# Performance work log

Hardware: AMD Instinct MI355X
Metric: run time of the kernel (lower is better)

The kernel has to match this reference:

```python
import jax, jax.numpy as jnp
import numpy as np

MAX_FREQ = 4
OMEGA = 0.5 * np.pi
PATCH = 64


def _unnorm(c, size):
    # align_corners=False convention of torch.grid_sample
    return ((c + 1.0) * size - 1.0) / 2.0


def _gather(im, yy, xx):
    # im [C,H,W], yy/xx [Ho,Wo] -> [C,Ho,Wo]
    return im[:, yy, xx]


def _gs_nearest(inp, grid):
    # inp [B,C,H,W], grid [B,Ho,Wo,2] (x,y); padding_mode='border'
    B, C, H, W = inp.shape
    x = jnp.clip(jnp.round(_unnorm(grid[..., 0], W)), 0, W - 1).astype(jnp.int32)
    y = jnp.clip(jnp.round(_unnorm(grid[..., 1], H)), 0, H - 1).astype(jnp.int32)
    return jax.vmap(_gather)(inp, y, x)  # [B,C,Ho,Wo]


def _gs_bilinear(inp, grid):
    B, C, H, W = inp.shape
    x = jnp.clip(_unnorm(grid[..., 0], W), 0.0, W - 1.0)
    y = jnp.clip(_unnorm(grid[..., 1], H), 0.0, H - 1.0)
    x0 = jnp.floor(x); y0 = jnp.floor(y)
    wx = (x - x0)[:, None]; wy = (y - y0)[:, None]  # [B,1,Ho,Wo]
    x0i = x0.astype(jnp.int32); y0i = y0.astype(jnp.int32)
    x1i = jnp.minimum(x0i + 1, W - 1); y1i = jnp.minimum(y0i + 1, H - 1)
    g = jax.vmap(_gather)
    v00 = g(inp, y0i, x0i); v01 = g(inp, y0i, x1i)
    v10 = g(inp, y1i, x0i); v11 = g(inp, y1i, x1i)
    return (v00 * (1 - wx) * (1 - wy) + v01 * wx * (1 - wy)
            + v10 * (1 - wx) * wy + v11 * wx * wy)


def _conv2d(x, w, b):
    y = jax.lax.conv_general_dilated(x, w, (1, 1), ((1, 1), (1, 1)),
                                     dimension_numbers=("NCHW", "OIHW", "NCHW"))
    return y + b[None, :, None, None]


def _lc_decoder(q, rel):
    # q [B,Ho,Wo,2F+1], rel [B,Ho,Wo,1]; Fourier basis [1, cos(k*w*rel), sin(k*w*rel)]
    k = jnp.arange(1, MAX_FREQ + 1, dtype=q.dtype)
    ang = rel * k * OMEGA  # [B,Ho,Wo,F]
    basis = jnp.concatenate([jnp.ones_like(rel), jnp.cos(ang), jnp.sin(ang)], axis=-1)
    return jnp.sum(q * basis, axis=-1, keepdims=True)  # [B,Ho,Wo,1]


def _forward(sinogram, feat, grid, square_inv, adapt_w, adapt_b):
    B = feat.shape[0]
    sino = _conv2d(feat, adapt_w, adapt_b)          # [B,2F+1,V,D]
    V, D = sino.shape[-2], sino.shape[-1]
    # make_coord along detector axis (dim=1 coord channel), padding=0
    coord_d = ((jnp.arange(D, dtype=sino.dtype) + 0.5) / D) * 2.0 - 1.0
    sino_coord = jnp.broadcast_to(coord_d[None, None, None, :], (B, 1, V, D))
    shift_interval = 1.0 / D
    eps = 1e-4
    q_recons, lengths = [], []
    for sx in (-shift_interval, shift_interval):  # ensembling shifts
        g = grid + jnp.array([sx, 0.0], dtype=grid.dtype) + 1e-6
        q_recon = jnp.transpose(_gs_nearest(sino, g), (0, 2, 3, 1))       # [B,V,P2,2F+1]
        q_coord = jnp.transpose(_gs_nearest(sino_coord, g), (0, 2, 3, 1))  # [B,V,P2,1]
        rel = (grid[..., 0:1] - q_coord) * D
        q_recons.append(_lc_decoder(q_recon, rel))
        lengths.append(jnp.abs(rel) + eps)
    tot = lengths[0] + lengths[1]
    # lengths are swapped before weighting (cross weighting)
    recon = q_recons[0] * lengths[1] / tot + q_recons[1] * lengths[0] / tot
    out = jnp.sum(jnp.transpose(recon, (0, 3, 1, 2)) * square_inv * 10000.0, axis=-2)
    # back projection of center channel of raw sinogram
    ch = sinogram.shape[1]
    bp = _gs_bilinear(sinogram[:, ch // 2:ch // 2 + 1], grid)
    out = out + jnp.sum(bp * square_inv * 10000.0, axis=-2)  # [B,1,P2]
    return out.reshape(B, 1, PATCH, PATCH)


def setup_inputs() -> dict:
    key = jax.random.key(0)
    ks = jax.random.split(key, 6)
    B, V, D, ENC = 4, 360, 512, 64
    P2 = PATCH * PATCH
    CH = 2 * MAX_FREQ + 1
    return {
        "sinogram": jax.random.normal(ks[0], (B, 1, V, D), jnp.float32),
        "feat": jax.random.normal(ks[1], (B, ENC, V, D), jnp.float32),
        "grid": jax.random.uniform(ks[2], (B, V, P2, 2), jnp.float32, -1.0, 1.0),
        "square_inv": jax.random.uniform(ks[3], (B, 1, V, P2), jnp.float32, 1e-5, 1e-4),
        "adapt_w": jax.random.normal(ks[4], (CH, ENC, 3, 3), jnp.float32) * 0.05,
        "adapt_b": jax.random.normal(ks[5], (CH,), jnp.float32) * 0.05,
    }


def reference(sinogram, feat, grid, square_inv, adapt_w, adapt_b):
    return _forward(sinogram, feat, grid, square_inv, adapt_w, adapt_b)
```

## Files before the change

kernel.cpp:

```cpp
#include <hip/hip_runtime.h>
#include <math.h>

#define B   4
#define V   360
#define D   512
#define ENC 64
#define CH  9
#define P2  4096
#define NCHUNK 24
#define VCHUNK 15
#define DPT 4

template <int SS>
__global__ __launch_bounds__(256) void conv_kernel(
    const float* __restrict__ feat,
    const float* __restrict__ w,
    const float* __restrict__ bias,
    float* __restrict__ sino)
{
    const int bid = blockIdx.x;
    const int sw  = (bid & 7) * 90 + (bid >> 3);
    const int b   = sw / 180;
    const int vt  = sw % 180;
    const int tr  = threadIdx.x >> 7;
    const int v   = vt * 2 + tr;
    const int d0  = (threadIdx.x & 127) * DPT;

    float acc[CH][DPT];
    #pragma unroll
    for (int oc = 0; oc < CH; ++oc) {
        const float bv = bias[oc];
        #pragma unroll
        for (int p = 0; p < DPT; ++p) acc[oc][p] = bv;
    }

    const float* fb = feat + ((size_t)b * ENC * V + v) * D + d0;
    const bool vm = v > 0, vp = v < V - 1;
    const bool dm = d0 > 0, dp = (d0 + DPT) < D;

    for (int ic = 0; ic < ENC; ++ic) {
        const float* f = fb + (size_t)ic * (V * D);
        float r[3][DPT + 2];
        #pragma unroll
        for (int rr = 0; rr < 3; ++rr) {
            const float* fr = f + (rr - 1) * D;
            const bool ok = (rr == 0) ? vm : ((rr == 2) ? vp : true);
            float4 c = ok ? *(const float4*)fr : float4{0.f, 0.f, 0.f, 0.f};
            r[rr][1] = c.x; r[rr][2] = c.y; r[rr][3] = c.z; r[rr][4] = c.w;
            r[rr][0] = (ok && dm) ? fr[-1]  : 0.f;
            r[rr][5] = (ok && dp) ? fr[DPT] : 0.f;
        }
        #pragma unroll
        for (int oc = 0; oc < CH; ++oc) {
            const float* ww = w + ((size_t)oc * ENC + ic) * 9;
            #pragma unroll
            for (int kr = 0; kr < 3; ++kr) {
                #pragma unroll
                for (int kc = 0; kc < 3; ++kc) {
                    const float wv = ww[kr * 3 + kc];
                    #pragma unroll
                    for (int p = 0; p < DPT; ++p)
                        acc[oc][p] = fmaf(r[kr][p + kc], wv, acc[oc][p]);
                }
            }
        }
    }

    #pragma unroll
    for (int p = 0; p < DPT; ++p) {
        float* so = sino + (size_t)(((size_t)b * V + v) * D + d0 + p) * SS;
        if (SS == 16) {
            float4* so4 = (float4*)so;
            so4[0] = float4{acc[0][p], acc[1][p], acc[2][p], acc[3][p]};
            so4[1] = float4{acc[4][p], acc[5][p], acc[6][p], acc[7][p]};
            so[8]  = acc[8][p];
        } else {
            #pragma unroll
            for (int oc = 0; oc < CH; ++oc) so[oc] = acc[oc][p];
        }
    }
}

template <int SS>
__global__ __launch_bounds__(256) void sample_kernel(
    const float* __restrict__ sino,
    const float* __restrict__ sinogram,
    const float* __restrict__ grid,
    const float* __restrict__ sq,
    float* __restrict__ partial)
{
    const int p  = blockIdx.x * 256 + threadIdx.x;
    const int v0 = blockIdx.y * VCHUNK;
    const int b  = blockIdx.z;

    const float* sg = sinogram + (size_t)b * V * D;
    const float* sb = sino + (size_t)b * V * D * SS;

    float acc = 0.f;
    for (int v = v0; v < v0 + VCHUNK; ++v) {
        const size_t gi = (size_t)(b * V + v) * P2 + p;
        const float gx = grid[gi * 2 + 0];
        const float gy = grid[gi * 2 + 1];
        const float s  = sq[gi];

        float fy = ((gy + 1e-6f + 1.f) * (float)V - 1.f) * 0.5f;
        int   yi = (int)fminf(fmaxf(rintf(fy), 0.f), (float)(V - 1));

        float val[2], len[2];
        #pragma unroll
        for (int sft = 0; sft < 2; ++sft) {
            const float sxv = (sft == 0) ? (-1.f / (float)D) : (1.f / (float)D);
            float fx = ((gx + sxv + 1e-6f + 1.f) * (float)D - 1.f) * 0.5f;
            int   xi = (int)fminf(fmaxf(rintf(fx), 0.f), (float)(D - 1));
            float qc = ((float)xi + 0.5f) * (2.f / (float)D) - 1.f;
            float rel = (gx - qc) * (float)D;

            float q[9];
            const float* qp = sb + (size_t)(yi * D + xi) * SS;
            if (SS == 16) {
                const float4* q4 = (const float4*)qp;
                float4 a = q4[0], c = q4[1];
                q[0] = a.x; q[1] = a.y; q[2] = a.z; q[3] = a.w;
                q[4] = c.x; q[5] = c.y; q[6] = c.z; q[7] = c.w;
                q[8] = qp[8];
            } else {
                #pragma unroll
                for (int k = 0; k < 9; ++k) q[k] = qp[k];
            }

            const float ang = rel * 1.5707963267948966f;
            float s1, c1;
            __sincosf(ang, &s1, &c1);
            const float c2 = fmaf(2.f * c1, c1, -1.f);
            const float s2 = 2.f * c1 * s1;
            const float c3 = fmaf(2.f * c1, c2, -c1);
            const float s3 = fmaf(2.f * c1, s2, -s1);
            const float c4 = fmaf(2.f * c1, c3, -c2);
            const float s4 = fmaf(2.f * c1, s3, -s2);

            float vv = q[0];
            vv = fmaf(q[1], c1, vv); vv = fmaf(q[2], c2, vv);
            vv = fmaf(q[3], c3, vv); vv = fmaf(q[4], c4, vv);
            vv = fmaf(q[5], s1, vv); vv = fmaf(q[6], s2, vv);
            vv = fmaf(q[7], s3, vv); vv = fmaf(q[8], s4, vv);
            val[sft] = vv;
            len[sft] = fabsf(rel) + 1e-4f;
        }
        const float tot   = len[0] + len[1];
        const float recon = (val[0] * len[1] + val[1] * len[0]) / tot;

        float fxb = fminf(fmaxf(((gx + 1.f) * (float)D - 1.f) * 0.5f, 0.f), (float)(D - 1));
        float fyb = fminf(fmaxf(((gy + 1.f) * (float)V - 1.f) * 0.5f, 0.f), (float)(V - 1));
        float x0 = floorf(fxb), y0 = floorf(fyb);
        float wx = fxb - x0,    wy = fyb - y0;
        int x0i = (int)x0, y0i = (int)y0;
        int x1i = min(x0i + 1, D - 1), y1i = min(y0i + 1, V - 1);
        float v00 = sg[y0i * D + x0i], v01 = sg[y0i * D + x1i];
        float v10 = sg[y1i * D + x0i], v11 = sg[y1i * D + x1i];
        float bp = v00 * (1.f - wx) * (1.f - wy) + v01 * wx * (1.f - wy)
                 + v10 * (1.f - wx) * wy        + v11 * wx * wy;

        acc += (recon + bp) * s * 1e4f;
    }
    partial[((size_t)blockIdx.y * B + b) * P2 + p] = acc;
}

__global__ __launch_bounds__(256) void reduce_kernel(
    const float* __restrict__ partial, float* __restrict__ out)
{
    const int i = blockIdx.x * 256 + threadIdx.x;
    float a = 0.f;
    #pragma unroll
    for (int c = 0; c < NCHUNK; ++c) a += partial[(size_t)c * B * P2 + i];
    out[i] = a;
}

extern "C" void kernel_launch(void* const* d_in, const int* in_sizes, int n_in,
                              void* d_out, int out_size, void* d_ws, size_t ws_size,
                              hipStream_t stream)
{
    const float* sinogram = (const float*)d_in[0];
    const float* feat     = (const float*)d_in[1];
    const float* grid     = (const float*)d_in[2];
    const float* sq       = (const float*)d_in[3];
    const float* w        = (const float*)d_in[4];
    const float* bias     = (const float*)d_in[5];
    float* out = (float*)d_out;

    const size_t part_bytes = (size_t)NCHUNK * B * P2 * sizeof(float);
    const size_t need16 = (size_t)B * V * D * 16 * sizeof(float) + part_bytes;
    const int ss = (ws_size >= need16) ? 16 : 9;

    float* sino    = (float*)d_ws;
    float* partial = (float*)((char*)d_ws + (size_t)B * V * D * ss * sizeof(float));

    dim3 sgrid(P2 / 256, NCHUNK, B);
    if (ss == 16) {
        conv_kernel<16><<<dim3(720), 256, 0, stream>>>(feat, w, bias, sino);
        sample_kernel<16><<<sgrid, 256, 0, stream>>>(sino, sinogram, grid, sq, partial);
    } else {
        conv_kernel<9><<<dim3(720), 256, 0, stream>>>(feat, w, bias, sino);
        sample_kernel<9><<<sgrid, 256, 0, stream>>>(sino, sinogram, grid, sq, partial);
    }

    reduce_kernel<<<dim3((B * P2) / 256), 256, 0, stream>>>(partial, out);
}
```

Measured before the change: 314.5 us.

## Store conv output as fp16 records and remap sample grid per XCD

The conv kernel now has each thread compute 8 detector columns over 4 views per block, and it writes its 9 channels as packed fp16 in a 32-byte record instead of fp32. The sample kernel reads these half records, loads grid coordinates as a single 64-bit nontemporal load, and processes two views per iteration. It also uses a new block index mapping that keeps each batch on a pair of XCDs, with a smaller view chunk and therefore more partial sums. The goal is to cut gather bandwidth and cache pressure in the sampling stage and raise parallelism. The cost is lower precision of the intermediate sinogram features, which could affect accuracy tolerance.

```diff
diff --git a/kernel.cpp b/kernel.cpp
--- a/kernel.cpp
+++ b/kernel.cpp
@@ -1,4 +1,5 @@
 #include <hip/hip_runtime.h>
+#include <hip/hip_fp16.h>
 #include <math.h>
 
 #define B   4
@@ -7,24 +8,24 @@
 #define ENC 64
 #define CH  9
 #define P2  4096
-#define NCHUNK 24
-#define VCHUNK 15
-#define DPT 4
-
-template <int SS>
+#define NCHUNK 45
+#define VCHUNK 8
+#define DPT 8
+#define RECH 16
+
 __global__ __launch_bounds__(256) void conv_kernel(
     const float* __restrict__ feat,
     const float* __restrict__ w,
     const float* __restrict__ bias,
-    float* __restrict__ sino)
+    __half* __restrict__ sino)
 {
     const int bid = blockIdx.x;
-    const int sw  = (bid & 7) * 90 + (bid >> 3);
-    const int b   = sw / 180;
-    const int vt  = sw % 180;
-    const int tr  = threadIdx.x >> 7;
-    const int v   = vt * 2 + tr;
-    const int d0  = (threadIdx.x & 127) * DPT;
+    const int sw  = (bid & 7) * 45 + (bid >> 3);
+    const int b   = sw / 90;
+    const int vt  = sw % 90;
+    const int tr  = threadIdx.x >> 6;
+    const int v   = vt * 4 + tr;
+    const int d0  = (threadIdx.x & 63) * DPT;
 
     float acc[CH][DPT];
     #pragma unroll
@@ -45,10 +46,12 @@
         for (int rr = 0; rr < 3; ++rr) {
             const float* fr = f + (rr - 1) * D;
             const bool ok = (rr == 0) ? vm : ((rr == 2) ? vp : true);
-            float4 c = ok ? *(const float4*)fr : float4{0.f, 0.f, 0.f, 0.f};
-            r[rr][1] = c.x; r[rr][2] = c.y; r[rr][3] = c.z; r[rr][4] = c.w;
-            r[rr][0] = (ok && dm) ? fr[-1]  : 0.f;
-            r[rr][5] = (ok && dp) ? fr[DPT] : 0.f;
+            float4 c0 = ok ? *(const float4*)fr       : float4{0.f, 0.f, 0.f, 0.f};
+            float4 c1 = ok ? *(const float4*)(fr + 4) : float4{0.f, 0.f, 0.f, 0.f};
+            r[rr][1] = c0.x; r[rr][2] = c0.y; r[rr][3] = c0.z; r[rr][4] = c0.w;
+            r[rr][5] = c1.x; r[rr][6] = c1.y; r[rr][7] = c1.z; r[rr][8] = c1.w;
+            r[rr][0]       = (ok && dm) ? fr[-1]   : 0.f;
+            r[rr][DPT + 1] = (ok && dp) ? fr[DPT]  : 0.f;
         }
         #pragma unroll
         for (int oc = 0; oc < CH; ++oc) {
@@ -68,101 +71,123 @@
 
     #pragma unroll
     for (int p = 0; p < DPT; ++p) {
-        float* so = sino + (size_t)(((size_t)b * V + v) * D + d0 + p) * SS;
-        if (SS == 16) {
-            float4* so4 = (float4*)so;
-            so4[0] = float4{acc[0][p], acc[1][p], acc[2][p], acc[3][p]};
-            so4[1] = float4{acc[4][p], acc[5][p], acc[6][p], acc[7][p]};
-            so[8]  = acc[8][p];
-        } else {
-            #pragma unroll
-            for (int oc = 0; oc < CH; ++oc) so[oc] = acc[oc][p];
-        }
-    }
-}
-
-template <int SS>
+        __half* rec = sino + (size_t)(((size_t)b * V + v) * D + d0 + p) * RECH;
+        union { __half2 h; unsigned u; } cv;
+        uint4 pk;
+        cv.h = __floats2half2_rn(acc[0][p], acc[1][p]); pk.x = cv.u;
+        cv.h = __floats2half2_rn(acc[2][p], acc[3][p]); pk.y = cv.u;
+        cv.h = __floats2half2_rn(acc[4][p], acc[5][p]); pk.z = cv.u;
+        cv.h = __floats2half2_rn(acc[6][p], acc[7][p]); pk.w = cv.u;
+        *(uint4*)rec = pk;
+        cv.h = __floats2half2_rn(acc[8][p], 0.f);
+        *(unsigned*)(rec + 8) = cv.u;
+    }
+}
+
+__device__ __forceinline__ void unpack9(const __half* rec, float* q)
+{
+    const uint4 a = *(const uint4*)rec;
+    union { unsigned u; __half2 h; } c;
+    float2 f;
+    c.u = a.x; f = __half22float2(c.h); q[0] = f.x; q[1] = f.y;
+    c.u = a.y; f = __half22float2(c.h); q[2] = f.x; q[3] = f.y;
+    c.u = a.z; f = __half22float2(c.h); q[4] = f.x; q[5] = f.y;
+    c.u = a.w; f = __half22float2(c.h); q[6] = f.x; q[7] = f.y;
+    const unsigned e = *(const unsigned*)(rec + 8);
+    union { unsigned short us; __half hh; } c2;
+    c2.us = (unsigned short)e;
+    q[8] = __half2float(c2.hh);
+}
+
+__device__ __forceinline__ float point_contrib(
+    int b, int v, int p,
+    const __half* __restrict__ sb, const float* __restrict__ sg,
+    const float* __restrict__ grid, const float* __restrict__ sq)
+{
+    const size_t gi = (size_t)(b * V + v) * P2 + p;
+    const double gd = __builtin_nontemporal_load((const double*)grid + gi);
+    const unsigned long long gu = __double_as_longlong(gd);
+    const float gx = __uint_as_float((unsigned)gu);
+    const float gy = __uint_as_float((unsigned)(gu >> 32));
+    const float s  = __builtin_nontemporal_load(sq + gi);
+
+    const float fy = ((gy + 1e-6f + 1.f) * (float)V - 1.f) * 0.5f;
+    const int   yi = (int)fminf(fmaxf(rintf(fy), 0.f), (float)(V - 1));
+    const float fx0 = ((gx + 1e-6f + 1.f) * (float)D - 1.f) * 0.5f;
+
+    float val[2], len[2];
+    #pragma unroll
+    for (int sft = 0; sft < 2; ++sft) {
+        const float fx = (sft == 0) ? (fx0 - 0.5f) : (fx0 + 0.5f);
+        const int   xi = (int)fminf(fmaxf(rintf(fx), 0.f), (float)(D - 1));
+        const float qc = ((float)xi + 0.5f) * (2.f / (float)D) - 1.f;
+        const float rel = (gx - qc) * (float)D;
+
+        float q[9];
+        unpack9(sb + (size_t)(yi * D + xi) * RECH, q);
+
+        const float ang = rel * 1.5707963267948966f;
+        float s1, c1;
+        __sincosf(ang, &s1, &c1);
+        const float c2 = fmaf(2.f * c1, c1, -1.f);
+        const float s2 = 2.f * c1 * s1;
+        const float c3 = fmaf(2.f * c1, c2, -c1);
+        const float s3 = fmaf(2.f * c1, s2, -s1);
+        const float c4 = fmaf(2.f * c1, c3, -c2);
+        const float s4 = fmaf(2.f * c1, s3, -s2);
+
+        float vv = q[0];
+        vv = fmaf(q[1], c1, vv); vv = fmaf(q[2], c2, vv);
+        vv = fmaf(q[3], c3, vv); vv = fmaf(q[4], c4, vv);
+        vv = fmaf(q[5], s1, vv); vv = fmaf(q[6], s2, vv);
+        vv = fmaf(q[7], s3, vv); vv = fmaf(q[8], s4, vv);
+        val[sft] = vv;
+        len[sft] = fabsf(rel) + 1e-4f;
+    }
+    const float tot   = len[0] + len[1];
+    const float recon = (val[0] * len[1] + val[1] * len[0]) / tot;
+
+    float fxb = fminf(fmaxf(((gx + 1.f) * (float)D - 1.f) * 0.5f, 0.f), (float)(D - 1));
+    float fyb = fminf(fmaxf(((gy + 1.f) * (float)V - 1.f) * 0.5f, 0.f), (float)(V - 1));
+    const float x0 = floorf(fxb), y0 = floorf(fyb);
+    const float wx = fxb - x0,    wy = fyb - y0;
+    const int x0i = (int)x0, y0i = (int)y0;
+    const int x1i = min(x0i + 1, D - 1), y1i = min(y0i + 1, V - 1);
+    const float v00 = sg[y0i * D + x0i], v01 = sg[y0i * D + x1i];
+    const float v10 = sg[y1i * D + x0i], v11 = sg[y1i * D + x1i];
+    const float bp = v00 * (1.f - wx) * (1.f - wy) + v01 * wx * (1.f - wy)
+                   + v10 * (1.f - wx) * wy        + v11 * wx * wy;
+
+    return (recon + bp) * s * 1e4f;
+}
+
 __global__ __launch_bounds__(256) void sample_kernel(
-    const float* __restrict__ sino,
+    const __half* __restrict__ sino,
     const float* __restrict__ sinogram,
     const float* __restrict__ grid,
     const float* __restrict__ sq,
     float* __restrict__ partial)
 {
-    const int p  = blockIdx.x * 256 + threadIdx.x;
-    const int v0 = blockIdx.y * VCHUNK;
-    const int b  = blockIdx.z;
+    const int bid = blockIdx.x;
+    const int xcd = bid & 7;
+    const int b   = xcd >> 1;
+    const int idx = ((bid >> 3) << 1) | (xcd & 1);
+    const int chunk = idx >> 4;
+    const int p  = (idx & 15) * 256 + threadIdx.x;
+    const int v0 = chunk * VCHUNK;
 
     const float* sg = sinogram + (size_t)b * V * D;
-    const float* sb = sino + (size_t)b * V * D * SS;
+    const __half* sb = sino + (size_t)b * V * D * RECH;
 
     float acc = 0.f;
-    for (int v = v0; v < v0 + VCHUNK; ++v) {
-        const size_t gi = (size_t)(b * V + v) * P2 + p;
-        const float gx = grid[gi * 2 + 0];
-        const float gy = grid[gi * 2 + 1];
-        const float s  = sq[gi];
-
-        float fy = ((gy + 1e-6f + 1.f) * (float)V - 1.f) * 0.5f;
-        int   yi = (int)fminf(fmaxf(rintf(fy), 0.f), (float)(V - 1));
-
-        float val[2], len[2];
-        #pragma unroll
-        for (int sft = 0; sft < 2; ++sft) {
-            const float sxv = (sft == 0) ? (-1.f / (float)D) : (1.f / (float)D);
-            float fx = ((gx + sxv + 1e-6f + 1.f) * (float)D - 1.f) * 0.5f;
-            int   xi = (int)fminf(fmaxf(rintf(fx), 0.f), (float)(D - 1));
-            float qc = ((float)xi + 0.5f) * (2.f / (float)D) - 1.f;
-            float rel = (gx - qc) * (float)D;
-
-            float q[9];
-            const float* qp = sb + (size_t)(yi * D + xi) * SS;
-            if (SS == 16) {
-                const float4* q4 = (const float4*)qp;
-                float4 a = q4[0], c = q4[1];
-                q[0] = a.x; q[1] = a.y; q[2] = a.z; q[3] = a.w;
-                q[4] = c.x; q[5] = c.y; q[6] = c.z; q[7] = c.w;
-                q[8] = qp[8];
-            } else {
-                #pragma unroll
-                for (int k = 0; k < 9; ++k) q[k] = qp[k];
-            }
-
-            const float ang = rel * 1.5707963267948966f;
-            float s1, c1;
-            __sincosf(ang, &s1, &c1);
-            const float c2 = fmaf(2.f * c1, c1, -1.f);
-            const float s2 = 2.f * c1 * s1;
-            const float c3 = fmaf(2.f * c1, c2, -c1);
-            const float s3 = fmaf(2.f * c1, s2, -s1);
-            const float c4 = fmaf(2.f * c1, c3, -c2);
-            const float s4 = fmaf(2.f * c1, s3, -s2);
-
-            float vv = q[0];
-            vv = fmaf(q[1], c1, vv); vv = fmaf(q[2], c2, vv);
-            vv = fmaf(q[3], c3, vv); vv = fmaf(q[4], c4, vv);
-            vv = fmaf(q[5], s1, vv); vv = fmaf(q[6], s2, vv);
-            vv = fmaf(q[7], s3, vv); vv = fmaf(q[8], s4, vv);
-            val[sft] = vv;
-            len[sft] = fabsf(rel) + 1e-4f;
-        }
-        const float tot   = len[0] + len[1];
-        const float recon = (val[0] * len[1] + val[1] * len[0]) / tot;
-
-        float fxb = fminf(fmaxf(((gx + 1.f) * (float)D - 1.f) * 0.5f, 0.f), (float)(D - 1));
-        float fyb = fminf(fmaxf(((gy + 1.f) * (float)V - 1.f) * 0.5f, 0.f), (float)(V - 1));
-        float x0 = floorf(fxb), y0 = floorf(fyb);
-        float wx = fxb - x0,    wy = fyb - y0;
-        int x0i = (int)x0, y0i = (int)y0;
-        int x1i = min(x0i + 1, D - 1), y1i = min(y0i + 1, V - 1);
-        float v00 = sg[y0i * D + x0i], v01 = sg[y0i * D + x1i];
-        float v10 = sg[y1i * D + x0i], v11 = sg[y1i * D + x1i];
-        float bp = v00 * (1.f - wx) * (1.f - wy) + v01 * wx * (1.f - wy)
-                 + v10 * (1.f - wx) * wy        + v11 * wx * wy;
-
-        acc += (recon + bp) * s * 1e4f;
-    }
-    partial[((size_t)blockIdx.y * B + b) * P2 + p] = acc;
+    #pragma unroll 1
+    for (int v = v0; v < v0 + VCHUNK; v += 2) {
+        const float c0 = point_contrib(b, v,     p, sb, sg, grid, sq);
+        const float c1 = point_contrib(b, v + 1, p, sb, sg, grid, sq);
+        acc += c0;
+        acc += c1;
+    }
+    __builtin_nontemporal_store(acc, partial + ((size_t)chunk * B + b) * P2 + p);
 }
 
 __global__ __launch_bounds__(256) void reduce_kernel(
@@ -171,7 +196,8 @@
     const int i = blockIdx.x * 256 + threadIdx.x;
     float a = 0.f;
     #pragma unroll
-    for (int c = 0; c < NCHUNK; ++c) a += partial[(size_t)c * B * P2 + i];
+    for (int c = 0; c < NCHUNK; ++c)
+        a += __builtin_nontemporal_load(partial + (size_t)c * B * P2 + i);
     out[i] = a;
 }
 
@@ -187,21 +213,10 @@
     const float* bias     = (const float*)d_in[5];
     float* out = (float*)d_out;
 
-    const size_t part_bytes = (size_t)NCHUNK * B * P2 * sizeof(float);
-    const size_t need16 = (size_t)B * V * D * 16 * sizeof(float) + part_bytes;
-    const int ss = (ws_size >= need16) ? 16 : 9;
-
-    float* sino    = (float*)d_ws;
-    float* partial = (float*)((char*)d_ws + (size_t)B * V * D * ss * sizeof(float));
-
-    dim3 sgrid(P2 / 256, NCHUNK, B);
-    if (ss == 16) {
-        conv_kernel<16><<<dim3(720), 256, 0, stream>>>(feat, w, bias, sino);
-        sample_kernel<16><<<sgrid, 256, 0, stream>>>(sino, sinogram, grid, sq, partial);
-    } else {
-        conv_kernel<9><<<dim3(720), 256, 0, stream>>>(feat, w, bias, sino);
-        sample_kernel<9><<<sgrid, 256, 0, stream>>>(sino, sinogram, grid, sq, partial);
-    }
-
+    __half* sino    = (__half*)d_ws;
+    float*  partial = (float*)((char*)d_ws + (size_t)B * V * D * RECH * sizeof(__half));
+
+    conv_kernel<<<dim3(360), 256, 0, stream>>>(feat, w, bias, sino);
+    sample_kernel<<<dim3(2880), 256, 0, stream>>>(sino, sinogram, grid, sq, partial);
     reduce_kernel<<<dim3((B * P2) / 256), 256, 0, stream>>>(partial, out);
 }
```

New measurement: 297.4 us. 5.4% less time.
